# Kernel optimization log

Hardware: AMD Instinct MI355X
Metric: run time of the kernel (lower is better)

## Reference

```python
import jax, jax.numpy as jnp
from jax import lax
import numpy as np

CH = 16
STAGES = 6
DN = ('NDHWC', 'DHWIO', 'NDHWC')


def setup_inputs() -> dict:
    key = jax.random.key(0)
    ks = jax.random.split(key, 16)
    B, G = 8, 64
    x = jax.random.normal(ks[0], (B, G, G, G, 1), dtype=jnp.float32)
    mask = jax.random.randint(ks[1], (B, G, G, G), 0, 2, dtype=jnp.int32)
    meta = jax.random.normal(ks[2], (B, 3), dtype=jnp.float32)
    sched = jax.random.normal(ks[3], (B, 128), dtype=jnp.float32)
    s = 0.05
    w_stem = jax.random.normal(ks[4], (5, 5, 5, 1, CH), dtype=jnp.float32) * s
    w_stages = jax.random.normal(ks[5], (STAGES, 3, 3, 3, CH, CH), dtype=jnp.float32) * s
    meta_w1 = jax.random.normal(ks[6], (3, 32), dtype=jnp.float32) * s
    meta_b1 = jnp.zeros((32,), jnp.float32)
    meta_w2 = jax.random.normal(ks[7], (32, 16), dtype=jnp.float32) * s
    meta_b2 = jnp.zeros((16,), jnp.float32)
    mat_w = jax.random.normal(ks[8], (CH * STAGES + 16, 128), dtype=jnp.float32) * s
    mat_b = jnp.zeros((128,), jnp.float32)
    sch_w = jax.random.normal(ks[9], (128, 128), dtype=jnp.float32) * s
    sch_b = jnp.zeros((128,), jnp.float32)
    f1_w = jax.random.normal(ks[10], (256, 128), dtype=jnp.float32) * s
    f1_b = jnp.zeros((128,), jnp.float32)
    f2_w = jax.random.normal(ks[11], (128, 1), dtype=jnp.float32) * s
    f2_b = jnp.zeros((1,), jnp.float32)
    return dict(x=x, mask=mask, meta=meta, sched=sched, w_stem=w_stem,
                w_stages=w_stages, meta_w1=meta_w1, meta_b1=meta_b1,
                meta_w2=meta_w2, meta_b2=meta_b2, mat_w=mat_w, mat_b=mat_b,
                sch_w=sch_w, sch_b=sch_b, f1_w=f1_w, f1_b=f1_b,
                f2_w=f2_w, f2_b=f2_b)


def _pool_mask(m):
    # ME stride-2 output coords = unique(coords // 2): 2x2x2 max-pool, ceil sizes
    return lax.reduce_window(m, jnp.float32(0), lax.max,
                             (1, 2, 2, 2), (1, 2, 2, 2), 'SAME')


def reference(x, mask, meta, sched, w_stem, w_stages, meta_w1, meta_b1,
              meta_w2, meta_b2, mat_w, mat_b, sch_w, sch_b,
              f1_w, f1_b, f2_w, f2_b):
    m = mask.astype(x.dtype)
    feats = x * m[..., None]                       # zero features off-mask
    y = lax.conv_general_dilated(feats, w_stem, (1, 1, 1), 'SAME',
                                 dimension_numbers=DN)
    y = jnp.maximum(y * m[..., None], 0.0)         # stem: conv + mask + ReLU
    pools = []
    for i in range(STAGES):
        y = lax.conv_general_dilated(y, w_stages[i], (2, 2, 2),
                                     [(1, 1), (1, 1), (1, 1)],
                                     dimension_numbers=DN)
        m = _pool_mask(m)
        y = jnp.maximum(y * m[..., None], 0.0)
        denom = jnp.maximum(m.sum(axis=(1, 2, 3)), 1.0)   # occupied voxels
        pools.append(y.sum(axis=(1, 2, 3)) / denom[:, None])
    pools = jnp.concatenate(pools, axis=1)                 # [B, CH*STAGES]
    h = jax.nn.relu(meta[:, :3] @ meta_w1 + meta_b1)
    meta_emb = h @ meta_w2 + meta_b2                        # [B,16]
    m_emb = jax.nn.relu(jnp.concatenate([pools, meta_emb], 1) @ mat_w + mat_b)
    s_emb = jax.nn.relu(sched @ sch_w + sch_b)
    z = jnp.concatenate([m_emb, s_emb], axis=1)             # [B,256]
    z = jax.nn.relu(z @ f1_w + f1_b)
    return z @ f2_w + f2_b                                  # [B,1]
```

## Files before the change

kernel.cpp:

```cpp
#include <hip/hip_runtime.h>

#define CH 16
#define NB 8

typedef unsigned short u16;
typedef unsigned char u8;
typedef unsigned int u32;
typedef __attribute__((ext_vector_type(8))) short s16x8;
typedef __attribute__((ext_vector_type(4))) float f32x4;

__device__ __forceinline__ float bflo(u32 u) { return __uint_as_float(u << 16); }
__device__ __forceinline__ float bfhi(u32 u) { return __uint_as_float(u & 0xffff0000u); }
__device__ __forceinline__ u32 bfrnd(float f) {
  u32 u = __float_as_uint(f);
  return (u + 0x7fffu + ((u >> 16) & 1u)) >> 16;
}
__device__ __forceinline__ u32 packbf_hw(float lo, float hi) {
  u32 r;
  asm("v_cvt_pk_bf16_f32 %0, %1, %2" : "=v"(r) : "v"(lo), "v"(hi));
  return r;
}

__global__ __launch_bounds__(256) void bprep_kernel(
    const float* __restrict__ w_stg, const float* __restrict__ w_stem,
    u16* __restrict__ bpre)
{
  const int e = blockIdx.x * 256 + (int)threadIdx.x;
  if (e >= 4 * 7168 + 3584) return;
  if (e < 4 * 7168) {
    const int s = e / 7168, r0 = e % 7168;
    const int i = r0 >> 9;
    const int r = r0 & 511;
    const int l = r >> 3, j = r & 7;
    const int tap = 2 * i + (l >> 5);
    const int cin = ((l >> 4) & 1) * 8 + j;
    const int n = l & 15;
    const float* w = w_stg + s * 27 * 256;
    const float val = (tap < 27) ? w[(tap * 16 + cin) * 16 + n] : 0.f;
    bpre[s * 7168 + i * 512 + l * 8 + j] = (u16)bfrnd(val);
  } else {
    const int e2 = e - 4 * 7168;
    const int i = e2 >> 9;
    const int r0 = e2 & 511;
    const int lane = r0 >> 3, j = r0 & 7;
    const int quad = lane >> 4, n = lane & 15;
    const int r = i * 4 + quad;
    const float val = (r < 25 && j < 5) ? w_stem[(r * 5 + j) * 16 + n] : 0.f;
    bpre[4 * 7168 + e2] = (u16)bfrnd(val);
  }
}

__global__ __launch_bounds__(256, 6) void stem_mfma(
    const float* __restrict__ x, const int* __restrict__ mask,
    const u16* __restrict__ bpre, u16* __restrict__ yout,
    float* __restrict__ pool_sum, float* __restrict__ cnt)
{
  __shared__ u16 cp[8 * 1168];

  const int b = blockIdx.y;
  const int u = blockIdx.x;
  const int tb = ((u & 7) << 6) | (u >> 3);
  const int z0 = (tb >> 6) * 8;
  const int y0 = ((tb >> 3) & 7) * 8;
  const int x0 = (tb & 7) * 8;
  const int tid = threadIdx.x;

  if (tb == 0) {
    if (tid < 96) pool_sum[b * 96 + tid] = 0.f;
    else if (tid < 102) cnt[b * 6 + (tid - 96)] = 0.f;
  }

  const int lane = tid & 63;
  const int wv = tid >> 6;
  const int n = lane & 15;
  const int quad = lane >> 4;
  const int vy = n >> 2, vx = n & 3;

  s16x8 wf[7];
  {
    const s16x8* wfp = (const s16x8*)(bpre + 4 * 7168);
#pragma unroll
    for (int i = 0; i < 7; ++i) wf[i] = wfp[i * 64 + lane];
  }

  if (tid < 144) {
    const int lz = tid / 12, ly = tid - lz * 12;
    const int gz = z0 + lz - 2, gy = y0 + ly - 2;
    uint4* dst = (uint4*)&cp[tid * 8];
    if ((unsigned)gz < 64u && (unsigned)gy < 64u) {
      const long long rowg =
          ((long long)((b * 64 + gz) * 64 + gy)) * 64 + (x0 - 2);
      float v[12];
      if (rowg >= 0 && rowg + 12 <= (long long)NB * 64 * 64 * 64) {
        const float2* xp = (const float2*)(x + rowg);
        const int2* mp2 = (const int2*)(mask + rowg);
        float2 xv[6]; int2 mv2[6];
#pragma unroll
        for (int j = 0; j < 6; ++j) { xv[j] = xp[j]; mv2[j] = mp2[j]; }
#pragma unroll
        for (int j = 0; j < 6; ++j) {
          v[2 * j]     = xv[j].x * (float)mv2[j].x;
          v[2 * j + 1] = xv[j].y * (float)mv2[j].y;
        }
        if (x0 == 0)  { v[0] = 0.f;  v[1] = 0.f;  }
        if (x0 == 56) { v[10] = 0.f; v[11] = 0.f; }
      } else {
#pragma unroll
        for (int j = 0; j < 12; ++j) {
          const int gx = x0 - 2 + j;
          float vv = 0.f;
          if ((unsigned)gx < 64u) {
            const long long gi = rowg + j;
            vv = x[gi] * (float)mask[gi];
          }
          v[j] = vv;
        }
      }
      const u32 c0 = packbf_hw(v[0], v[1]);
      const u32 c1 = packbf_hw(v[2], v[3]);
      const u32 c2 = packbf_hw(v[4], v[5]);
      const u32 c3 = packbf_hw(v[6], v[7]);
      const u32 c4 = packbf_hw(v[8], v[9]);
      const u32 c5 = packbf_hw(v[10], v[11]);
      const u32 d0 = packbf_hw(v[1], v[2]);
      const u32 d1 = packbf_hw(v[3], v[4]);
      const u32 d2 = packbf_hw(v[5], v[6]);
      const u32 d3 = packbf_hw(v[7], v[8]);
      const u32 d4 = packbf_hw(v[9], v[10]);
      const u32 d5 = packbf_hw(v[11], 0.f);
      dst[0 * 146] = make_uint4(c0, c1, c2, c3);
      dst[1 * 146] = make_uint4(d0, d1, d2, d3);
      dst[2 * 146] = make_uint4(c1, c2, c3, c4);
      dst[3 * 146] = make_uint4(d1, d2, d3, d4);
      dst[4 * 146] = make_uint4(c2, c3, c4, c5);
      dst[5 * 146] = make_uint4(d2, d3, d4, d5);
      dst[6 * 146] = make_uint4(c3, c4, c5, 0u);
      dst[7 * 146] = make_uint4(d3, d4, d5, 0u);
    } else {
#pragma unroll
      for (int p = 0; p < 8; ++p) dst[p * 146] = make_uint4(0u, 0u, 0u, 0u);
    }
  }
  __syncthreads();

  int doff[7];
#pragma unroll
  for (int i = 0; i < 7; ++i) {
    const int r = i * 4 + quad;
    doff[i] = (r < 25) ? ((r / 5) * 12 + (r % 5)) * 8 : 0;
  }
  const int base0 = vx * 1168 + (wv * 12 + vy) * 8;
  const int gi0 = ((b * 64 + z0 + wv) * 64 + y0 + vy) * 64 + x0 + vx;
  u16* outp = yout + (size_t)gi0 * 16 + quad * 4;

  float mvc = (float)mask[gi0];
  for (int s = 0; s < 8; ++s) {
    const int sz = (s >> 2) * 4, sy2 = ((s >> 1) & 1) * 4, sx = (s & 1) * 4;
    const int off = sz * 4096 + sy2 * 64 + sx;
    float mvn = 0.f;
    if (s < 7) {
      const int s1 = s + 1;
      const int offn = ((s1 >> 2) * 4) * 4096 + (((s1 >> 1) & 1) * 4) * 64 +
                       (s1 & 1) * 4;
      mvn = (float)mask[gi0 + offn];
    }
    const int base = base0 + sx * 1168 + (sz * 12 + sy2) * 8;
    f32x4 accA = {0.f, 0.f, 0.f, 0.f};
    f32x4 accB = {0.f, 0.f, 0.f, 0.f};
#pragma unroll
    for (int i = 0; i < 7; ++i) {
      const s16x8 bf = *(const s16x8*)&cp[base + doff[i]];
      if (i & 1)
        accB = __builtin_amdgcn_mfma_f32_16x16x32_bf16(wf[i], bf, accB, 0, 0, 0);
      else
        accA = __builtin_amdgcn_mfma_f32_16x16x32_bf16(wf[i], bf, accA, 0, 0, 0);
    }
    const float f0 = fmaxf(accA[0] + accB[0], 0.f) * mvc;
    const float f1 = fmaxf(accA[1] + accB[1], 0.f) * mvc;
    const float f2 = fmaxf(accA[2] + accB[2], 0.f) * mvc;
    const float f3 = fmaxf(accA[3] + accB[3], 0.f) * mvc;
    *(uint2*)(outp + (size_t)off * 16) =
        make_uint2(packbf_hw(f0, f1), packbf_hw(f2, f3));
    mvc = mvn;
  }
}

template <int S>
__global__ __launch_bounds__(256) void stage_mfma4(
    const u16* __restrict__ yin, const u16* __restrict__ bpre,
    const int* __restrict__ m_in_i, const u8* __restrict__ m_in_u8,
    u16* __restrict__ yout, u8* __restrict__ m_out,
    float* __restrict__ pool_sum, float* __restrict__ cnt,
    const int stage)
{
  __shared__ u16 lb[14 * 512];
  __shared__ float lC[4 * 16 * 17];
  __shared__ float lmp[256];

  constexpr int So = S >> 1;
  constexpr int nvox = So * So * So;
  constexpr int NBX = nvox / 256;
  const int b = blockIdx.y;
  const int tid = threadIdx.x;
  const int u = blockIdx.x;
  int bxi;
  if constexpr (NBX >= 8) bxi = (u & 7) * (NBX / 8) + (u >> 3);
  else bxi = u;
  const int vg0 = bxi * 256;

  {
    const uint4* src = (const uint4*)bpre;
    uint4* dst = (uint4*)lb;
    for (int e = tid; e < 896; e += 256) dst[e] = src[e];
  }

  {
    const int vox = vg0 + tid;
    const int oz = vox / (So * So);
    const int oy = (vox / So) % So;
    const int ox = vox % So;
    float mp = 0.f;
#pragma unroll
    for (int dz = 0; dz < 2; ++dz)
#pragma unroll
      for (int dy = 0; dy < 2; ++dy)
#pragma unroll
        for (int dx = 0; dx < 2; ++dx) {
          const int mi =
              ((b * S + 2 * oz + dz) * S + 2 * oy + dy) * S + 2 * ox + dx;
          const float mv = m_in_i ? (float)m_in_i[mi] : (float)m_in_u8[mi];
          mp = fmaxf(mp, mv);
        }
    lmp[tid] = mp;
  }
  __syncthreads();

  const int wv = tid >> 6;
  const int lane = tid & 63;
  const int m = lane & 15;
  const int quad = lane >> 4;
  const int qh = quad >> 1;
  const int qlo = quad & 1;

  int izb[4], iyb[4], ixb[4];
#pragma unroll
  for (int g = 0; g < 4; ++g) {
    const int vox = vg0 + wv * 64 + g * 16 + m;
    const int oz = vox / (So * So);
    const int oy = (vox / So) % So;
    const int ox = vox % So;
    izb[g] = 2 * oz - 1;
    iyb[g] = 2 * oy - 1;
    ixb[g] = 2 * ox - 1;
  }

  const s16x8* lbv = (const s16x8*)lb;
  f32x4 acc[4];
#pragma unroll
  for (int g = 0; g < 4; ++g) acc[g] = (f32x4){0.f, 0.f, 0.f, 0.f};

#pragma unroll
  for (int i = 0; i < 14; ++i) {
    const int t0 = 2 * i, t1 = 2 * i + 1;
    const int dz0 = t0 / 9, dy0 = (t0 / 3) % 3, dx0 = t0 % 3;
    const int dz1 = (t1 < 27) ? t1 / 9 : 1;
    const int dy1 = (t1 < 27) ? (t1 / 3) % 3 : 1;
    const int dx1 = (t1 < 27) ? t1 % 3 : 1;
    const int dzq = qh ? dz1 : dz0;
    const int dyq = qh ? dy1 : dy0;
    const int dxq = qh ? dx1 : dx0;

    uint4 ar[4];
#pragma unroll
    for (int g = 0; g < 4; ++g) {
      const int iz = izb[g] + dzq;
      const int iy = iyb[g] + dyq;
      const int ix = ixb[g] + dxq;
      const bool valid = (unsigned)iz < (unsigned)S &&
                         (unsigned)iy < (unsigned)S &&
                         (unsigned)ix < (unsigned)S;
      const int izc = min(max(iz, 0), S - 1);
      const int iyc = min(max(iy, 0), S - 1);
      const int ixc = min(max(ix, 0), S - 1);
      const size_t addr =
          (size_t)(((b * S + izc) * S + iyc) * S + ixc) * 16 + qlo * 8;
      uint4 v = *(const uint4*)(yin + addr);
      v.x = valid ? v.x : 0u;
      v.y = valid ? v.y : 0u;
      v.z = valid ? v.z : 0u;
      v.w = valid ? v.w : 0u;
      ar[g] = v;
    }
    const s16x8 bfrag = lbv[i * 64 + lane];
#pragma unroll
    for (int g = 0; g < 4; ++g)
      acc[g] = __builtin_amdgcn_mfma_f32_16x16x32_bf16(
          __builtin_bit_cast(s16x8, ar[g]), bfrag, acc[g], 0, 0, 0);
  }

  float psum = 0.f;
#pragma unroll
  for (int g = 0; g < 4; ++g) {
    __syncthreads();
    {
      float* lCw = lC + wv * 272;
      const int n = lane & 15;
#pragma unroll
      for (int reg = 0; reg < 4; ++reg) {
        const int row = quad * 4 + reg;
        lCw[row * 17 + n] =
            fmaxf(acc[g][reg], 0.f) * lmp[wv * 64 + g * 16 + row];
      }
    }
    __syncthreads();
    {
      const int vox_l = tid >> 2;
      const int cg = (tid & 3) * 4;
      const float* src = lC + (vox_l >> 4) * 272 + (vox_l & 15) * 17 + cg;
      const float f0 = src[0], f1 = src[1], f2 = src[2], f3 = src[3];
      const int lv = (vox_l >> 4) * 64 + g * 16 + (vox_l & 15);
      const size_t gi = (size_t)b * nvox + vg0 + lv;
      uint2* op = (uint2*)(yout + gi * 16 + cg);
      op[0] = make_uint2(packbf_hw(f0, f1), packbf_hw(f2, f3));
      if ((tid & 3) == 0) m_out[gi] = (u8)lmp[lv];
    }
    if (tid < 16) {
      float s = 0.f;
#pragma unroll 16
      for (int v = 0; v < 64; ++v)
        s += lC[(v >> 4) * 272 + (v & 15) * 17 + tid];
      psum += s;
    }
  }
  if (tid < 16) {
    atomicAdd(&pool_sum[(b * 6 + stage) * 16 + tid], psum);
  } else if (tid == 16) {
    float c = 0.f;
#pragma unroll 16
    for (int v = 0; v < 256; ++v) c += lmp[v];
    atomicAdd(&cnt[b * 6 + stage], c);
  }
}

__global__ __launch_bounds__(256) void tail_kernel(
    const u16* __restrict__ y3g, const u8* __restrict__ m3g,
    const u16* __restrict__ bpre,
    const float* __restrict__ wstg,
    const float* __restrict__ meta, const float* __restrict__ sched,
    const float* __restrict__ mw1, const float* __restrict__ mb1,
    const float* __restrict__ mw2, const float* __restrict__ mb2,
    const float* __restrict__ matw, const float* __restrict__ matb,
    const float* __restrict__ schw, const float* __restrict__ schb,
    const float* __restrict__ f1w, const float* __restrict__ f1b,
    const float* __restrict__ f2w, const float* __restrict__ f2b,
    const float* __restrict__ pool_sum, const float* __restrict__ cnt,
    float* __restrict__ out)
{
  const int b = blockIdx.x;
  const int t = threadIdx.x;
  __shared__ u16 ty3[8192];
  __shared__ float lm3[512];
  __shared__ float pb[4 * 64 * 17];
  __shared__ float ly4[64 * 16];
  __shared__ float lm4[64];
  __shared__ float ps4[256];
  __shared__ float ly5[8 * 16];
  __shared__ float lm5[8];
  __shared__ float ps5[128];
  __shared__ float lsum[3][16];
  __shared__ float lcnt[3];
  __shared__ float invec[112];
  __shared__ float hbuf[32];
  __shared__ float zbuf[256];
  __shared__ float psf[256];
  __shared__ float part[2];

  {
    const uint4* yb = (const uint4*)(y3g + (size_t)b * 8192);
    uint4* dst = (uint4*)ty3;
    for (int i = t; i < 1024; i += 256) dst[i] = yb[i];
    for (int i = t; i < 512; i += 256) lm3[i] = (float)m3g[b * 512 + i];
  }
  __syncthreads();

  {
    const int lane = t & 63;
    const int wv = t >> 6;
    const int mm = lane & 15;
    const int quad = lane >> 4;
    const int qh = quad >> 1, qlo = quad & 1;

    int iz0[4], iy0[4], ix0[4];
#pragma unroll
    for (int g = 0; g < 4; ++g) {
      const int vox = g * 16 + mm;
      iz0[g] = 2 * (vox >> 4) - 1;
      iy0[g] = 2 * ((vox >> 2) & 3) - 1;
      ix0[g] = 2 * (vox & 3) - 1;
    }
    f32x4 a3[4];
#pragma unroll
    for (int g = 0; g < 4; ++g) a3[g] = (f32x4){0.f, 0.f, 0.f, 0.f};
    const s16x8* bp3 = (const s16x8*)(bpre + 3 * 7168);
#pragma unroll
    for (int ii = 0; ii < 4; ++ii) {
      const int i = wv * 4 + ii;
      if (i < 14) {
        const int t0 = 2 * i, t1 = 2 * i + 1;
        const int dz0 = t0 / 9, dy0 = (t0 / 3) % 3, dx0 = t0 % 3;
        const int dz1 = (t1 < 27) ? t1 / 9 : 1;
        const int dy1 = (t1 < 27) ? (t1 / 3) % 3 : 1;
        const int dx1 = (t1 < 27) ? t1 % 3 : 1;
        const int dzq = qh ? dz1 : dz0;
        const int dyq = qh ? dy1 : dy0;
        const int dxq = qh ? dx1 : dx0;
        uint4 ar[4];
#pragma unroll
        for (int g = 0; g < 4; ++g) {
          const int iz = iz0[g] + dzq;
          const int iy = iy0[g] + dyq;
          const int ix = ix0[g] + dxq;
          const bool valid = (unsigned)iz < 8u && (unsigned)iy < 8u &&
                             (unsigned)ix < 8u;
          const int izc = min(max(iz, 0), 7);
          const int iyc = min(max(iy, 0), 7);
          const int ixc = min(max(ix, 0), 7);
          const int ad = ((izc * 8 + iyc) * 8 + ixc) * 16 + qlo * 8;
          uint4 v = *(const uint4*)&ty3[ad];
          v.x = valid ? v.x : 0u;
          v.y = valid ? v.y : 0u;
          v.z = valid ? v.z : 0u;
          v.w = valid ? v.w : 0u;
          ar[g] = v;
        }
        const s16x8 bf = bp3[i * 64 + lane];
#pragma unroll
        for (int g = 0; g < 4; ++g)
          a3[g] = __builtin_amdgcn_mfma_f32_16x16x32_bf16(
              __builtin_bit_cast(s16x8, ar[g]), bf, a3[g], 0, 0, 0);
      }
    }
#pragma unroll
    for (int g = 0; g < 4; ++g)
#pragma unroll
      for (int reg = 0; reg < 4; ++reg)
        pb[wv * 1088 + (g * 16 + quad * 4 + reg) * 17 + mm] = a3[g][reg];
  }
  __syncthreads();

  {
    const int vox = t >> 2, cg = (t & 3) * 4;
    const int oz = vox >> 4, oy = (vox >> 2) & 3, ox = vox & 3;
    float mp = 0.f;
#pragma unroll
    for (int dz = 0; dz < 2; ++dz)
#pragma unroll
      for (int dy = 0; dy < 2; ++dy)
#pragma unroll
        for (int dx = 0; dx < 2; ++dx)
          mp = fmaxf(mp, lm3[((2 * oz + dz) * 8 + 2 * oy + dy) * 8 +
                             2 * ox + dx]);
#pragma unroll
    for (int c = 0; c < 4; ++c) {
      const int ch = cg + c;
      const float s = pb[vox * 17 + ch] + pb[1088 + vox * 17 + ch] +
                      pb[2176 + vox * 17 + ch] + pb[3264 + vox * 17 + ch];
      ly4[vox * 16 + ch] = fmaxf(s, 0.f) * mp;
    }
    if (cg == 0) lm4[vox] = mp;
  }
  __syncthreads();

  if (t < 16) {
    float s = 0.f;
#pragma unroll 16
    for (int v = 0; v < 64; ++v) s += ly4[v * 16 + t];
    lsum[0][t] = s;
  } else if (t == 16) {
    float s = 0.f;
#pragma unroll 16
    for (int v = 0; v < 64; ++v) s += lm4[v];
    lcnt[0] = s;
  }
  {
    const float* w = wstg + 4 * 27 * 256;
    const int o = t >> 1, kh = t & 1;
    const int vox4 = o >> 4, co = o & 15;
    const int oz = vox4 >> 2, oy = (vox4 >> 1) & 1, ox = vox4 & 1;
    float acc = 0.f;
#pragma unroll
    for (int tt = 0; tt < 14; ++tt) {
      const int tap = tt + (kh ? 14 : 0);
      if (tap < 27) {
        const int dz = tap / 9, dy = (tap / 3) % 3, dx = tap % 3;
        const int iz = 2 * oz + dz - 1, iy = 2 * oy + dy - 1,
                  ix = 2 * ox + dx - 1;
        const float s = ((unsigned)iz < 4u && (unsigned)iy < 4u &&
                         (unsigned)ix < 4u) ? 1.f : 0.f;
        const int idx = ((min(max(iz, 0), 3) * 4 + min(max(iy, 0), 3)) * 4 +
                         min(max(ix, 0), 3)) * 16;
        const float* wp = w + tap * 256 + co;
#pragma unroll
        for (int ci = 0; ci < 16; ++ci)
          acc = fmaf(ly4[idx + ci] * s, wp[ci * 16], acc);
      }
    }
    ps4[t] = acc;
  }
  __syncthreads();

  if (t < 128) {
    const int vox4 = t >> 4, co = t & 15;
    float mp = 0.f;
#pragma unroll
    for (int dz = 0; dz < 2; ++dz)
#pragma unroll
      for (int dy = 0; dy < 2; ++dy)
#pragma unroll
        for (int dx = 0; dx < 2; ++dx)
          mp = fmaxf(mp, lm4[((2 * (vox4 >> 2) + dz) * 4 +
                              2 * ((vox4 >> 1) & 1) + dy) * 4 +
                             2 * (vox4 & 1) + dx]);
    ly5[t] = fmaxf(ps4[2 * t] + ps4[2 * t + 1], 0.f) * mp;
    if (co == 0) lm5[vox4] = mp;
  }
  __syncthreads();

  if (t < 16) {
    float s = 0.f;
#pragma unroll
    for (int v = 0; v < 8; ++v) s += ly5[v * 16 + t];
    lsum[1][t] = s;
  } else if (t == 16) {
    lcnt[1] = lm5[0] + lm5[1] + lm5[2] + lm5[3] + lm5[4] + lm5[5] + lm5[6] +
              lm5[7];
  }
  if (t < 128) {
    const float* w = wstg + 5 * 27 * 256;
    const int co = t & 15, k8 = t >> 4;
    float acc = 0.f;
#pragma unroll
    for (int tt = 0; tt < 4; ++tt) {
      const int tap = k8 * 4 + tt;
      if (tap < 27) {
        const int dz = tap / 9, dy = (tap / 3) % 3, dx = tap % 3;
        const int iz = dz - 1, iy = dy - 1, ix = dx - 1;
        const float s = ((unsigned)iz < 2u && (unsigned)iy < 2u &&
                         (unsigned)ix < 2u) ? 1.f : 0.f;
        const int idx = ((min(max(iz, 0), 1) * 2 + min(max(iy, 0), 1)) * 2 +
                         min(max(ix, 0), 1)) * 16;
        const float* wp = w + tap * 256 + co;
#pragma unroll
        for (int ci = 0; ci < 16; ++ci)
          acc = fmaf(ly5[idx + ci] * s, wp[ci * 16], acc);
      }
    }
    ps5[t] = acc;
  }
  __syncthreads();

  if (t < 16) {
    float s = ps5[t] + ps5[16 + t] + ps5[32 + t] + ps5[48 + t] +
              ps5[64 + t] + ps5[80 + t] + ps5[96 + t] + ps5[112 + t];
    float mp = 0.f;
#pragma unroll
    for (int v = 0; v < 8; ++v) mp = fmaxf(mp, lm5[v]);
    lsum[2][t] = fmaxf(s, 0.f) * mp;
    if (t == 0) lcnt[2] = mp;
  } else if (t >= 96 && t < 128) {
    const int j = t - 96;
    float h = mb1[j];
#pragma unroll
    for (int k = 0; k < 3; ++k) h = fmaf(meta[b * 3 + k], mw1[k * 32 + j], h);
    hbuf[j] = fmaxf(h, 0.f);
  }
  __syncthreads();

  if (t < 48) {
    const int s = t >> 4;
    invec[t] = pool_sum[b * 96 + t] / fmaxf(cnt[b * 6 + s], 1.f);
  } else if (t < 96) {
    const int s = (t >> 4) - 3;
    invec[t] = lsum[s][t & 15] / fmaxf(lcnt[s], 1.f);
  } else if (t < 112) {
    const int j = t - 96;
    float e = mb2[j];
#pragma unroll
    for (int k = 0; k < 32; ++k) e = fmaf(hbuf[k], mw2[k * 16 + j], e);
    invec[t] = e;
  }
  __syncthreads();

  if (t < 128) {
    float a = matb[t];
#pragma unroll 16
    for (int k = 0; k < 112; ++k) a = fmaf(invec[k], matw[k * 128 + t], a);
    zbuf[t] = fmaxf(a, 0.f);
  } else {
    const int c = t - 128;
    float s = schb[c];
#pragma unroll 16
    for (int k = 0; k < 128; ++k)
      s = fmaf(sched[b * 128 + k], schw[k * 128 + c], s);
    zbuf[128 + c] = fmaxf(s, 0.f);
  }
  __syncthreads();

  {
    const int col = t & 127, kh = t >> 7;
    float a = 0.f;
#pragma unroll 16
    for (int kk = 0; kk < 128; ++kk) {
      const int k = kh * 128 + kk;
      a = fmaf(zbuf[k], f1w[k * 128 + col], a);
    }
    psf[t] = a;
  }
  __syncthreads();

  if (t < 128) {
    const float a = psf[t] + psf[128 + t] + f1b[t];
    float v = fmaxf(a, 0.f) * f2w[t];
#pragma unroll
    for (int off = 32; off > 0; off >>= 1) v += __shfl_xor(v, off, 64);
    if ((t & 63) == 0) part[t >> 6] = v;
  }
  __syncthreads();
  if (t == 0) out[b] = part[0] + part[1] + f2b[0];
}

extern "C" void kernel_launch(void* const* d_in, const int* in_sizes, int n_in,
                              void* d_out, int out_size, void* d_ws,
                              size_t ws_size, hipStream_t stream)
{
  (void)in_sizes; (void)n_in; (void)out_size; (void)ws_size;
  const float* x      = (const float*)d_in[0];
  const int*   mask   = (const int*)  d_in[1];
  const float* meta   = (const float*)d_in[2];
  const float* sched  = (const float*)d_in[3];
  const float* w_stem = (const float*)d_in[4];
  const float* w_stg  = (const float*)d_in[5];
  const float* mw1    = (const float*)d_in[6];
  const float* mb1    = (const float*)d_in[7];
  const float* mw2    = (const float*)d_in[8];
  const float* mb2    = (const float*)d_in[9];
  const float* matw   = (const float*)d_in[10];
  const float* matb   = (const float*)d_in[11];
  const float* schw   = (const float*)d_in[12];
  const float* schb   = (const float*)d_in[13];
  const float* f1w    = (const float*)d_in[14];
  const float* f1b    = (const float*)d_in[15];
  const float* f2w    = (const float*)d_in[16];
  const float* f2b    = (const float*)d_in[17];
  float* out = (float*)d_out;

  char* ws = (char*)d_ws;
  size_t off = 0;
  auto alloc = [&](size_t nbytes) -> void* {
    void* p = ws + off;
    off += (nbytes + 255) & ~(size_t)255;
    return p;
  };

  u16* y0 = (u16*)alloc((size_t)NB * 64 * 64 * 64 * CH * 2);
  u16* y1 = (u16*)alloc((size_t)NB * 32 * 32 * 32 * CH * 2);
  u16* y2 = (u16*)alloc((size_t)NB * 16 * 16 * 16 * CH * 2);
  u16* y3 = (u16*)alloc((size_t)NB * 8 * 8 * 8 * CH * 2);
  u8* m1 = (u8*)alloc((size_t)NB * 32 * 32 * 32);
  u8* m2 = (u8*)alloc((size_t)NB * 16 * 16 * 16);
  u8* m3 = (u8*)alloc((size_t)NB * 8 * 8 * 8);
  float* pool_sum = (float*)alloc((NB * 96 + NB * 6) * 4);
  float* cnt = pool_sum + NB * 96;
  u16* bpre = (u16*)alloc((4 * 7168 + 3584) * 2);

  bprep_kernel<<<126, 256, 0, stream>>>(w_stg, w_stem, bpre);

  stem_mfma<<<dim3(512, NB), 256, 0, stream>>>(x, mask, bpre, y0,
                                               pool_sum, cnt);

  stage_mfma4<64><<<dim3(128, NB), 256, 0, stream>>>(
      y0, bpre + 0 * 7168, mask, (const u8*)nullptr, y1, m1,
      pool_sum, cnt, 0);
  stage_mfma4<32><<<dim3(16, NB), 256, 0, stream>>>(
      y1, bpre + 1 * 7168, (const int*)nullptr, m1, y2, m2,
      pool_sum, cnt, 1);
  stage_mfma4<16><<<dim3(2, NB), 256, 0, stream>>>(
      y2, bpre + 2 * 7168, (const int*)nullptr, m2, y3, m3,
      pool_sum, cnt, 2);

  tail_kernel<<<NB, 256, 0, stream>>>(y3, m3, bpre, w_stg, meta, sched,
                                      mw1, mb1, mw2, mb2, matw, matb,
                                      schw, schb, f1w, f1b, f2w, f2b,
                                      pool_sum, cnt, out);
}
```

Measured before the change: 196.8 us.

## Stage input halo tiles in LDS for strided stage convs with transposed MFMA

Replaces the per-tap global gathers in the strided stage convolutions with a cooperative load of a 3D input halo tile, split by channel half and stored in LDS in parity-split x layout. Each wave then reads im2col fragments from LDS. Weights become the A operand, prepacked in a new layout so that tap-major K groups line up with voxel columns. The output epilogue writes directly from registers and reduces the pool sums with wave shuffles instead of an LDS transpose, and the mask write is moved earlier. The cost is about 44KB of LDS per block, which limits occupancy, plus two load and sync phases per block.

Result: slower. 209.9 us (+6.7%).

```diff
diff --git a/kernel.cpp b/kernel.cpp
--- a/kernel.cpp
+++ b/kernel.cpp
@@ -2,6 +2,8 @@
 
 #define CH 16
 #define NB 8
+#define WOFF (4 * 7168 + 3584)
+#define WPRE_TOT (WOFF + 3 * 7168)
 
 typedef unsigned short u16;
 typedef unsigned char u8;
@@ -26,7 +28,7 @@
     u16* __restrict__ bpre)
 {
   const int e = blockIdx.x * 256 + (int)threadIdx.x;
-  if (e >= 4 * 7168 + 3584) return;
+  if (e >= WPRE_TOT) return;
   if (e < 4 * 7168) {
     const int s = e / 7168, r0 = e % 7168;
     const int i = r0 >> 9;
@@ -38,7 +40,7 @@
     const float* w = w_stg + s * 27 * 256;
     const float val = (tap < 27) ? w[(tap * 16 + cin) * 16 + n] : 0.f;
     bpre[s * 7168 + i * 512 + l * 8 + j] = (u16)bfrnd(val);
-  } else {
+  } else if (e < WOFF) {
     const int e2 = e - 4 * 7168;
     const int i = e2 >> 9;
     const int r0 = e2 & 511;
@@ -47,6 +49,20 @@
     const int r = i * 4 + quad;
     const float val = (r < 25 && j < 5) ? w_stem[(r * 5 + j) * 16 + n] : 0.f;
     bpre[4 * 7168 + e2] = (u16)bfrnd(val);
+  } else {
+    const int e3 = e - WOFF;
+    const int s = e3 / 7168;
+    const int r = e3 % 7168;
+    const int h = r / 3584;
+    const int r2 = r % 3584;
+    const int i = r2 >> 9;
+    const int l = (r2 >> 3) & 63;
+    const int j = r2 & 7;
+    const int quad = l >> 4, n = l & 15;
+    const int tap = i * 4 + quad;
+    const float val =
+        (tap < 27) ? w_stg[s * 6912 + tap * 256 + (h * 8 + j) * 16 + n] : 0.f;
+    bpre[WOFF + e3] = (u16)bfrnd(val);
   }
 }
 
@@ -186,39 +202,37 @@
 }
 
 template <int S>
-__global__ __launch_bounds__(256) void stage_mfma4(
+__global__ __launch_bounds__(256, 3) void stage_lds(
     const u16* __restrict__ yin, const u16* __restrict__ bpre,
     const int* __restrict__ m_in_i, const u8* __restrict__ m_in_u8,
     u16* __restrict__ yout, u8* __restrict__ m_out,
-    float* __restrict__ pool_sum, float* __restrict__ cnt,
-    const int stage)
+    float* __restrict__ pool_sum, float* __restrict__ cnt, const int stage)
 {
-  __shared__ u16 lb[14 * 512];
-  __shared__ float lC[4 * 16 * 17];
-  __shared__ float lmp[256];
-
   constexpr int So = S >> 1;
   constexpr int nvox = So * So * So;
-  constexpr int NBX = nvox / 256;
+  constexpr int NTX = So / 8;
+  constexpr int NTYX = (So / 8) * NTX;
+  __shared__ u16 din[2 * 9 * 17 * 9 * 8];
+  __shared__ float lmp[256];
+  __shared__ float lps[4][16];
+
   const int b = blockIdx.y;
   const int tid = threadIdx.x;
-  const int u = blockIdx.x;
   int bxi;
-  if constexpr (NBX >= 8) bxi = (u & 7) * (NBX / 8) + (u >> 3);
-  else bxi = u;
-  const int vg0 = bxi * 256;
+  if constexpr (S == 64) {
+    const int u = blockIdx.x;
+    bxi = (u & 7) * 16 + (u >> 3);
+  } else {
+    bxi = blockIdx.x;
+  }
+  const int tz = bxi / NTYX;
+  const int rem = bxi % NTYX;
+  const int ty = rem / NTX;
+  const int tx = rem % NTX;
 
   {
-    const uint4* src = (const uint4*)bpre;
-    uint4* dst = (uint4*)lb;
-    for (int e = tid; e < 896; e += 256) dst[e] = src[e];
-  }
-
-  {
-    const int vox = vg0 + tid;
-    const int oz = vox / (So * So);
-    const int oy = (vox / So) % So;
-    const int ox = vox % So;
+    const int ozl = tid >> 6, oyl = (tid >> 3) & 7, oxl = tid & 7;
+    const int oz = tz * 4 + ozl, oy = ty * 8 + oyl, ox = tx * 8 + oxl;
     float mp = 0.f;
 #pragma unroll
     for (int dz = 0; dz < 2; ++dz)
@@ -232,108 +246,106 @@
           mp = fmaxf(mp, mv);
         }
     lmp[tid] = mp;
-  }
-  __syncthreads();
-
+    m_out[(size_t)b * nvox + (oz * So + oy) * So + ox] = (u8)mp;
+  }
+
+  const int lane = tid & 63;
   const int wv = tid >> 6;
-  const int lane = tid & 63;
-  const int m = lane & 15;
+  const int n = lane & 15;
   const int quad = lane >> 4;
-  const int qh = quad >> 1;
-  const int qlo = quad & 1;
-
-  int izb[4], iyb[4], ixb[4];
-#pragma unroll
-  for (int g = 0; g < 4; ++g) {
-    const int vox = vg0 + wv * 64 + g * 16 + m;
-    const int oz = vox / (So * So);
-    const int oy = (vox / So) % So;
-    const int ox = vox % So;
-    izb[g] = 2 * oz - 1;
-    iyb[g] = 2 * oy - 1;
-    ixb[g] = 2 * ox - 1;
-  }
-
-  const s16x8* lbv = (const s16x8*)lb;
+
+  const int tbase = wv * 2448 + (n >> 3) * 144 + (n & 7) * 8;
+  int toff[7];
+#pragma unroll
+  for (int i = 0; i < 7; ++i) {
+    const int tap = i * 4 + quad;
+    if (tap < 27) {
+      const int dz = tap / 9, dy = (tap / 3) % 3, dx = tap % 3;
+      toff[i] = (dx & 1) * 11016 + dz * 1224 + dy * 72 + (dx >> 1) * 8;
+    } else {
+      toff[i] = 0;
+    }
+  }
+
   f32x4 acc[4];
 #pragma unroll
   for (int g = 0; g < 4; ++g) acc[g] = (f32x4){0.f, 0.f, 0.f, 0.f};
 
-#pragma unroll
-  for (int i = 0; i < 14; ++i) {
-    const int t0 = 2 * i, t1 = 2 * i + 1;
-    const int dz0 = t0 / 9, dy0 = (t0 / 3) % 3, dx0 = t0 % 3;
-    const int dz1 = (t1 < 27) ? t1 / 9 : 1;
-    const int dy1 = (t1 < 27) ? (t1 / 3) % 3 : 1;
-    const int dx1 = (t1 < 27) ? t1 % 3 : 1;
-    const int dzq = qh ? dz1 : dz0;
-    const int dyq = qh ? dy1 : dy0;
-    const int dxq = qh ? dx1 : dx0;
-
-    uint4 ar[4];
+  for (int h = 0; h < 2; ++h) {
+    __syncthreads();
+    for (int e = tid; e < 9 * 17 * 17; e += 256) {
+      const int izl = e / 289;
+      const int r = e - izl * 289;
+      const int iyl = r / 17;
+      const int ixl = r - iyl * 17;
+      const int giz = tz * 8 - 1 + izl;
+      const int giy = ty * 16 - 1 + iyl;
+      const int gix = tx * 16 - 1 + ixl;
+      uint4 v = make_uint4(0u, 0u, 0u, 0u);
+      if ((unsigned)giz < (unsigned)S && (unsigned)giy < (unsigned)S &&
+          (unsigned)gix < (unsigned)S) {
+        const size_t a =
+            ((size_t)(((b * S + giz) * S + giy) * S + gix)) * 16 + h * 8;
+        v = *(const uint4*)(yin + a);
+      }
+      *(uint4*)&din[((((ixl & 1) * 9 + izl) * 17 + iyl) * 9 + (ixl >> 1)) * 8] = v;
+    }
+    __syncthreads();
+
+    s16x8 wf[7];
+    {
+      const s16x8* wfp = (const s16x8*)(bpre + WOFF + stage * 7168 + h * 3584);
+#pragma unroll
+      for (int i = 0; i < 7; ++i) wf[i] = wfp[i * 64 + lane];
+    }
+#pragma unroll
+    for (int i = 0; i < 7; ++i) {
+      s16x8 bf[4];
+#pragma unroll
+      for (int g = 0; g < 4; ++g)
+        bf[g] = *(const s16x8*)&din[tbase + toff[i] + g * 288];
+#pragma unroll
+      for (int g = 0; g < 4; ++g)
+        acc[g] = __builtin_amdgcn_mfma_f32_16x16x32_bf16(wf[i], bf[g], acc[g],
+                                                         0, 0, 0);
+    }
+  }
+
+  {
+    const int gbase =
+        ((tz * 4 + wv) * So + ty * 8 + (n >> 3)) * So + tx * 8 + (n & 7);
+    float ps0 = 0.f, ps1 = 0.f, ps2 = 0.f, ps3 = 0.f;
 #pragma unroll
     for (int g = 0; g < 4; ++g) {
-      const int iz = izb[g] + dzq;
-      const int iy = iyb[g] + dyq;
-      const int ix = ixb[g] + dxq;
-      const bool valid = (unsigned)iz < (unsigned)S &&
-                         (unsigned)iy < (unsigned)S &&
-                         (unsigned)ix < (unsigned)S;
-      const int izc = min(max(iz, 0), S - 1);
-      const int iyc = min(max(iy, 0), S - 1);
-      const int ixc = min(max(ix, 0), S - 1);
-      const size_t addr =
-          (size_t)(((b * S + izc) * S + iyc) * S + ixc) * 16 + qlo * 8;
-      uint4 v = *(const uint4*)(yin + addr);
-      v.x = valid ? v.x : 0u;
-      v.y = valid ? v.y : 0u;
-      v.z = valid ? v.z : 0u;
-      v.w = valid ? v.w : 0u;
-      ar[g] = v;
-    }
-    const s16x8 bfrag = lbv[i * 64 + lane];
-#pragma unroll
-    for (int g = 0; g < 4; ++g)
-      acc[g] = __builtin_amdgcn_mfma_f32_16x16x32_bf16(
-          __builtin_bit_cast(s16x8, ar[g]), bfrag, acc[g], 0, 0, 0);
-  }
-
-  float psum = 0.f;
-#pragma unroll
-  for (int g = 0; g < 4; ++g) {
-    __syncthreads();
-    {
-      float* lCw = lC + wv * 272;
-      const int n = lane & 15;
-#pragma unroll
-      for (int reg = 0; reg < 4; ++reg) {
-        const int row = quad * 4 + reg;
-        lCw[row * 17 + n] =
-            fmaxf(acc[g][reg], 0.f) * lmp[wv * 64 + g * 16 + row];
-      }
-    }
-    __syncthreads();
-    {
-      const int vox_l = tid >> 2;
-      const int cg = (tid & 3) * 4;
-      const float* src = lC + (vox_l >> 4) * 272 + (vox_l & 15) * 17 + cg;
-      const float f0 = src[0], f1 = src[1], f2 = src[2], f3 = src[3];
-      const int lv = (vox_l >> 4) * 64 + g * 16 + (vox_l & 15);
-      const size_t gi = (size_t)b * nvox + vg0 + lv;
-      uint2* op = (uint2*)(yout + gi * 16 + cg);
-      op[0] = make_uint2(packbf_hw(f0, f1), packbf_hw(f2, f3));
-      if ((tid & 3) == 0) m_out[gi] = (u8)lmp[lv];
-    }
-    if (tid < 16) {
-      float s = 0.f;
-#pragma unroll 16
-      for (int v = 0; v < 64; ++v)
-        s += lC[(v >> 4) * 272 + (v & 15) * 17 + tid];
-      psum += s;
-    }
-  }
+      const int lv = wv * 64 + g * 16 + n;
+      const float mp = lmp[lv];
+      const float f0 = fmaxf(acc[g][0], 0.f) * mp;
+      const float f1 = fmaxf(acc[g][1], 0.f) * mp;
+      const float f2 = fmaxf(acc[g][2], 0.f) * mp;
+      const float f3 = fmaxf(acc[g][3], 0.f) * mp;
+      const size_t gi = (size_t)b * nvox + gbase + g * 2 * So;
+      *(uint2*)(yout + gi * 16 + quad * 4) =
+          make_uint2(packbf_hw(f0, f1), packbf_hw(f2, f3));
+      ps0 += f0; ps1 += f1; ps2 += f2; ps3 += f3;
+    }
+#pragma unroll
+    for (int m = 1; m < 16; m <<= 1) {
+      ps0 += __shfl_xor(ps0, m, 64);
+      ps1 += __shfl_xor(ps1, m, 64);
+      ps2 += __shfl_xor(ps2, m, 64);
+      ps3 += __shfl_xor(ps3, m, 64);
+    }
+    if (n == 0) {
+      lps[wv][quad * 4 + 0] = ps0;
+      lps[wv][quad * 4 + 1] = ps1;
+      lps[wv][quad * 4 + 2] = ps2;
+      lps[wv][quad * 4 + 3] = ps3;
+    }
+  }
+  __syncthreads();
   if (tid < 16) {
-    atomicAdd(&pool_sum[(b * 6 + stage) * 16 + tid], psum);
+    const float s = lps[0][tid] + lps[1][tid] + lps[2][tid] + lps[3][tid];
+    atomicAdd(&pool_sum[(b * 6 + stage) * 16 + tid], s);
   } else if (tid == 16) {
     float c = 0.f;
 #pragma unroll 16
@@ -671,22 +683,20 @@
   u8* m3 = (u8*)alloc((size_t)NB * 8 * 8 * 8);
   float* pool_sum = (float*)alloc((NB * 96 + NB * 6) * 4);
   float* cnt = pool_sum + NB * 96;
-  u16* bpre = (u16*)alloc((4 * 7168 + 3584) * 2);
-
-  bprep_kernel<<<126, 256, 0, stream>>>(w_stg, w_stem, bpre);
+  u16* bpre = (u16*)alloc((size_t)WPRE_TOT * 2);
+
+  bprep_kernel<<<(WPRE_TOT + 255) / 256, 256, 0, stream>>>(w_stg, w_stem,
+                                                           bpre);
 
   stem_mfma<<<dim3(512, NB), 256, 0, stream>>>(x, mask, bpre, y0,
                                                pool_sum, cnt);
 
-  stage_mfma4<64><<<dim3(128, NB), 256, 0, stream>>>(
-      y0, bpre + 0 * 7168, mask, (const u8*)nullptr, y1, m1,
-      pool_sum, cnt, 0);
-  stage_mfma4<32><<<dim3(16, NB), 256, 0, stream>>>(
-      y1, bpre + 1 * 7168, (const int*)nullptr, m1, y2, m2,
-      pool_sum, cnt, 1);
-  stage_mfma4<16><<<dim3(2, NB), 256, 0, stream>>>(
-      y2, bpre + 2 * 7168, (const int*)nullptr, m2, y3, m3,
-      pool_sum, cnt, 2);
+  stage_lds<64><<<dim3(128, NB), 256, 0, stream>>>(
+      y0, bpre, mask, (const u8*)nullptr, y1, m1, pool_sum, cnt, 0);
+  stage_lds<32><<<dim3(16, NB), 256, 0, stream>>>(
+      y1, bpre, (const int*)nullptr, m1, y2, m2, pool_sum, cnt, 1);
+  stage_lds<16><<<dim3(2, NB), 256, 0, stream>>>(
+      y2, bpre, (const int*)nullptr, m2, y3, m3, pool_sum, cnt, 2);
 
   tail_kernel<<<NB, 256, 0, stream>>>(y3, m3, bpre, w_stg, meta, sched,
                                       mw1, mb1, mw2, mb2, matw, matb,
```
